# Optimization experiments

Hardware: AMD Instinct MI355X
Metric: run time of the kernel (lower is better)

The kernel has to match this reference:

```python
import jax, jax.numpy as jnp
import numpy as np

L, D, H, F_IN = 3, 256, 8, 5
HD = D // H
FF = 4 * D
EPS = 1e-5


def _layer_norm(x, g, b):
    mu = jnp.mean(x, axis=-1, keepdims=True)
    var = jnp.mean(jnp.square(x - mu), axis=-1, keepdims=True)
    return (x - mu) * jax.lax.rsqrt(var + EPS) * g + b


def setup_inputs() -> dict:
    key = jax.random.key(0)
    ks = jax.random.split(key, 20)
    s = 0.02
    inp = {
        'x': jax.random.normal(ks[0], (32, 512, F_IN), jnp.float32),
        'mask': jax.random.randint(ks[1], (32, 512), 0, 2) == 1,
        'Win': jax.random.normal(ks[2], (F_IN, D), jnp.float32) * s,
        'bin_': jnp.zeros((D,), jnp.float32),
        'Wq': jax.random.normal(ks[3], (L, D, D), jnp.float32) * s,
        'bq': jnp.zeros((L, D), jnp.float32),
        'Wk': jax.random.normal(ks[4], (L, D, D), jnp.float32) * s,
        'bk': jnp.zeros((L, D), jnp.float32),
        'Wv': jax.random.normal(ks[5], (L, D, D), jnp.float32) * s,
        'bv': jnp.zeros((L, D), jnp.float32),
        'Wo': jax.random.normal(ks[6], (L, D, D), jnp.float32) * s,
        'bo': jnp.zeros((L, D), jnp.float32),
        'g1': jnp.ones((L, D), jnp.float32),
        'b1': jnp.zeros((L, D), jnp.float32),
        'W1': jax.random.normal(ks[7], (L, D, FF), jnp.float32) * s,
        'c1': jnp.zeros((L, FF), jnp.float32),
        'W2': jax.random.normal(ks[8], (L, FF, D), jnp.float32) * s,
        'c2': jnp.zeros((L, D), jnp.float32),
        'g2': jnp.ones((L, D), jnp.float32),
        'b2': jnp.zeros((L, D), jnp.float32),
    }
    return inp


def reference(x, mask, Win, bin_, Wq, bq, Wk, bk, Wv, bv, Wo, bo, g1, b1, W1, c1, W2, c2, g2, b2):
    B, S, _ = x.shape
    scale = 1.0 / jnp.sqrt(jnp.float32(HD))
    h = x @ Win + bin_  # [B,S,D]
    kmask = mask[:, None, None, :]  # [B,1,1,S] key-padding mask
    for l in range(L):
        q = (h @ Wq[l] + bq[l]).reshape(B, S, H, HD).transpose(0, 2, 1, 3)
        k = (h @ Wk[l] + bk[l]).reshape(B, S, H, HD).transpose(0, 2, 1, 3)
        v = (h @ Wv[l] + bv[l]).reshape(B, S, H, HD).transpose(0, 2, 1, 3)
        scores = jnp.einsum('bhqd,bhkd->bhqk', q, k) * scale
        scores = jnp.where(kmask, -jnp.inf, scores)
        attn = jnp.nan_to_num(jax.nn.softmax(scores, axis=-1), nan=0.0)
        ao = jnp.einsum('bhqk,bhkd->bhqd', attn, v).transpose(0, 2, 1, 3).reshape(B, S, D)
        ao = ao @ Wo[l] + bo[l]
        h = _layer_norm(h + ao, g1[l], b1[l])
        ff = jax.nn.relu(h @ W1[l] + c1[l]) @ W2[l] + c2[l]
        h = _layer_norm(h + ff, g2[l], b2[l])
    return h
```

## Files before the change

### kernel.cpp

```cpp
#include <hip/hip_runtime.h>
#include <cstdint>

#define NLAYER 3
#define DMODEL 256
#define NHEAD 8
#define HEADD 32
#define FFDIM 1024
#define BATCH 32
#define SEQ 512
#define MTOK (BATCH*SEQ)

typedef __attribute__((ext_vector_type(8))) __bf16 bf16x8;
typedef __attribute__((ext_vector_type(4))) __bf16 bf16x4;
typedef __attribute__((ext_vector_type(4))) float f32x4;
typedef __attribute__((ext_vector_type(16))) float f32x16;

typedef __attribute__((address_space(1))) const uint8_t ga_t;
typedef __attribute__((address_space(3))) uint8_t la_t;
__device__ __forceinline__ void gll16(const void* g, void* l) {
    __builtin_amdgcn_global_load_lds((ga_t*)g, (la_t*)l, 16, 0, 0);
}

__global__ __launch_bounds__(256)
void prep_kernel(const float* __restrict__ Wq, const float* __restrict__ Wk,
                 const float* __restrict__ Wv, const float* __restrict__ Wo,
                 const float* __restrict__ W1, const float* __restrict__ W2,
                 const float* __restrict__ bq, const float* __restrict__ bk,
                 const float* __restrict__ bv,
                 __bf16* __restrict__ wqf, __bf16* __restrict__ wot,
                 __bf16* __restrict__ w1f, __bf16* __restrict__ w2f,
                 float* __restrict__ bqkv,
                 const float* __restrict__ x, const float* __restrict__ Win,
                 const float* __restrict__ bin, __bf16* __restrict__ h16)
{
    const int bid = blockIdx.x;
    const int tid = threadIdx.x;
    if (bid >= 2313) {
        const int m0 = (bid - 2313) * 8;
        const float bv_ = bin[tid];
#pragma unroll
        for (int p = 0; p < 8; ++p) {
            const int m = m0 + p;
            const float* xr = x + (size_t)m * 5;
            float acc = bv_;
#pragma unroll
            for (int k = 0; k < 5; ++k) acc += xr[k] * Win[k * DMODEL + tid];
            h16[(size_t)m * DMODEL + tid] = (__bf16)acc;
        }
        return;
    }
    if (bid >= 3 * 768) {
        int idx = (bid - 3 * 768) * 256 + tid;
        int l = idx / 768, j = idx % 768;
        float v = (j < 256) ? bq[l * 256 + j]
                : (j < 512) ? bk[l * 256 + j - 256]
                            : bv[l * 256 + j - 512];
        bqkv[idx] = v;
        return;
    }
    const int l = bid / 768;
    const int rr = bid % 768;
    __shared__ float tile[32][33];
    const int c = tid & 31, rbase = tid >> 5;

    if (rr < 192) {
        const int ty = rr >> 6;
        const int t = rr & 63;
        const float* src = (ty == 0 ? Wq : ty == 1 ? Wk : Wv) + (size_t)l * 65536;
        const int tk = t >> 3, tj = t & 7;
#pragma unroll
        for (int p = 0; p < 4; ++p) {
            int kr = rbase + p * 8;
            tile[kr][c] = src[(size_t)(tk * 32 + kr) * 256 + tj * 32 + c];
        }
        __syncthreads();
        if (tid < 128) {
            const int lane = tid & 63, ksl = tid >> 6;
            const int cl = lane & 31, kh = lane >> 5;
            bf16x8 v;
#pragma unroll
            for (int j = 0; j < 8; ++j) v[j] = (__bf16)tile[ksl * 16 + kh * 8 + j][cl];
            *(bf16x8*)(wqf + ((size_t)(((l * 8 + tj) * 3 + ty) * 16
                              + tk * 2 + ksl)) * 512 + lane * 8) = v;
        }
        return;
    }
    if (rr < 256) {
        const int t = rr - 192;
        const float* src = Wo + (size_t)l * 65536;
        __bf16* dst = wot + (size_t)l * 65536;
        const int tk = t >> 3, tj = t & 7;
#pragma unroll
        for (int p = 0; p < 4; ++p) {
            int kr = rbase + p * 8;
            tile[kr][c] = src[(size_t)(tk * 32 + kr) * 256 + tj * 32 + c];
        }
        __syncthreads();
#pragma unroll
        for (int p = 0; p < 4; ++p) {
            int nr = rbase + p * 8;
            dst[(size_t)(tj * 32 + nr) * 256 + tk * 32 + c] = (__bf16)tile[c][nr];
        }
        return;
    }
    const float* src; __bf16* dst; int N, KT, t;
    if (rr < 512) { t = rr - 256; src = W1 + (size_t)l * 262144;
                    dst = w1f + (size_t)l * 262144; N = 1024; KT = 8; }
    else          { t = rr - 512; src = W2 + (size_t)l * 262144;
                    dst = w2f + (size_t)l * 262144; N = 256;  KT = 32; }
    const int tn = N >> 5;
    const int tk = t / tn, tj = t % tn;
#pragma unroll
    for (int p = 0; p < 4; ++p) {
        int kr = rbase + p * 8;
        tile[kr][c] = src[(size_t)(tk * 32 + kr) * N + tj * 32 + c];
    }
    __syncthreads();
    if (tid < 128) {
        const int l_n = tid >> 2, k8 = tid & 3;
        const int n = tj * 32 + l_n;
        bf16x8 v;
#pragma unroll
        for (int j = 0; j < 8; ++j) v[j] = (__bf16)tile[k8 * 8 + j][l_n];
        *(bf16x8*)(dst + ((size_t)((n >> 4) * KT + tk) * 64 + k8 * 16 + (n & 15)) * 8) = v;
    }
}

__global__ __launch_bounds__(1024)
void attn_kernel(const __bf16* __restrict__ hA, const __bf16* __restrict__ wqf,
                 const float* __restrict__ bqkv, const int* __restrict__ mask,
                 __bf16* __restrict__ ao)
{
    __shared__ __bf16 Ks[512 * 40];
    __shared__ __bf16 Vt[32 * 520];
    __shared__ __attribute__((aligned(16))) __bf16 Un[3*16*512];
    __shared__ float maskadd[512];

    const int b = blockIdx.x >> 3;
    const int h = blockIdx.x & 7;
    const int t = threadIdx.x;
    const int lane = t & 63;
    const int wave = t >> 6;
    const int cl = lane & 31;
    const int kh = lane >> 5;
    const float scale = 0.17677669529663687f;

    {
        const __bf16* wsrc = wqf + (size_t)h * 24576;
#pragma unroll
        for (int p = 0; p < 3; ++p) {
            const int chunk = p * 1024 + t;
            gll16(wsrc + (size_t)chunk * 8, Un + (p * 1024 + wave * 64) * 8);
        }
    }
    if (t < 512) maskadd[t] = mask[b * SEQ + t] ? -1e30f : 0.f;
    __syncthreads();

    const int tok0 = wave * 32;
    const size_t arow = ((size_t)(b * SEQ + tok0 + cl)) * 256;
    f32x16 aQ, aK, aV;
#pragma unroll
    for (int i = 0; i < 16; ++i) { aQ[i] = 0.f; aK[i] = 0.f; aV[i] = 0.f; }
#pragma unroll
    for (int ks = 0; ks < 16; ++ks) {
        bf16x8 tf = *(const bf16x8*)(hA + arow + ks * 16 + kh * 8);
        bf16x8 wq = *(const bf16x8*)(Un + (0 * 16 + ks) * 512 + lane * 8);
        bf16x8 wk = *(const bf16x8*)(Un + (1 * 16 + ks) * 512 + lane * 8);
        bf16x8 wv = *(const bf16x8*)(Un + (2 * 16 + ks) * 512 + lane * 8);
        aQ = __builtin_amdgcn_mfma_f32_32x32x16_bf16(wq, tf, aQ, 0, 0, 0);
        aK = __builtin_amdgcn_mfma_f32_32x32x16_bf16(wk, tf, aK, 0, 0, 0);
        aV = __builtin_amdgcn_mfma_f32_32x32x16_bf16(wv, tf, aV, 0, 0, 0);
    }
#pragma unroll
    for (int r = 0; r < 16; ++r) {
        const int rdim = (r & 3) + 8 * (r >> 2) + 4 * kh;
        Ks[(tok0 + cl) * 40 + rdim] = (__bf16)(aK[r] + bqkv[256 + h * 32 + rdim]);
        Vt[rdim * 520 + tok0 + cl]  = (__bf16)(aV[r] + bqkv[512 + h * 32 + rdim]);
    }
    __syncthreads();

    __bf16* Pw = Un + wave * 1024;
#pragma unroll
    for (int r = 0; r < 16; ++r) {
        const int rdim = (r & 3) + 8 * (r >> 2) + 4 * kh;
        Pw[cl * 32 + rdim] = (__bf16)(aQ[r] + bqkv[h * 32 + rdim]);
    }
    bf16x8 qf0 = *(const bf16x8*)(Pw + cl * 32 + kh * 8);
    bf16x8 qf1 = *(const bf16x8*)(Pw + cl * 32 + 16 + kh * 8);
    __syncthreads();

    f32x16 oacc;
#pragma unroll
    for (int i = 0; i < 16; ++i) oacc[i] = 0.f;
    float lsum = 0.f;

    for (int kt = 0; kt < SEQ; kt += 32) {
        bf16x8 kf0 = *(const bf16x8*)(Ks + (kt + cl) * 40 + kh * 8);
        bf16x8 kf1 = *(const bf16x8*)(Ks + (kt + cl) * 40 + 16 + kh * 8);
        f32x16 s;
#pragma unroll
        for (int i = 0; i < 16; ++i) s[i] = 0.f;
        s = __builtin_amdgcn_mfma_f32_32x32x16_bf16(kf0, qf0, s, 0, 0, 0);
        s = __builtin_amdgcn_mfma_f32_32x32x16_bf16(kf1, qf1, s, 0, 0, 0);
        float pv[16];
#pragma unroll
        for (int g = 0; g < 4; ++g) {
            f32x4 mv = *(const f32x4*)(maskadd + kt + 8 * g + 4 * kh);
#pragma unroll
            for (int r = 0; r < 4; ++r) {
                float e = __expf(s[g * 4 + r] * scale + mv[r]);
                pv[g * 4 + r] = e;
                lsum += e;
            }
        }
#pragma unroll
        for (int g = 0; g < 4; ++g) {
            bf16x4 pb;
#pragma unroll
            for (int r = 0; r < 4; ++r) pb[r] = (__bf16)pv[g * 4 + r];
            *(bf16x4*)(Pw + cl * 32 + 8 * g + 4 * kh) = pb;
        }
        bf16x8 pf0 = *(const bf16x8*)(Pw + cl * 32 + kh * 8);
        bf16x8 pf1 = *(const bf16x8*)(Pw + cl * 32 + 16 + kh * 8);
        bf16x8 vf0 = *(const bf16x8*)(Vt + cl * 520 + kt + kh * 8);
        bf16x8 vf1 = *(const bf16x8*)(Vt + cl * 520 + kt + 16 + kh * 8);
        oacc = __builtin_amdgcn_mfma_f32_32x32x16_bf16(vf0, pf0, oacc, 0, 0, 0);
        oacc = __builtin_amdgcn_mfma_f32_32x32x16_bf16(vf1, pf1, oacc, 0, 0, 0);
    }

    lsum += __shfl_xor(lsum, 32);
    const float inv = (lsum > 0.f) ? 1.f / lsum : 0.f;
    __bf16* orow = ao + (size_t)(b * SEQ + tok0 + cl) * DMODEL + h * 32;
#pragma unroll
    for (int g = 0; g < 4; ++g) {
        bf16x4 w;
#pragma unroll
        for (int r = 0; r < 4; ++r) w[r] = (__bf16)(oacc[g * 4 + r] * inv);
        *(bf16x4*)(orow + 8 * g + 4 * kh) = w;
    }
}

template<int LAST>
__global__ __launch_bounds__(256, 4)
void gemm_ln_kernel(const __bf16* __restrict__ A, const __bf16* __restrict__ Bt,
                    const float* __restrict__ bias, const __bf16* __restrict__ res,
                    const float* __restrict__ g, const float* __restrict__ be,
                    __bf16* __restrict__ out16, float* __restrict__ out32, int K)
{
    __shared__ __bf16 As[32 * 64];
    __shared__ __bf16 Bs[256 * 64];
    __shared__ float red[32 * 8];
    const int tid = threadIdx.x;
    const int m0 = blockIdx.x * 32;
    const int lane = tid & 63;
    const int wave = tid >> 6;
    const int wn = wave * 64;
    const int fr = lane & 15;
    const int quad = lane >> 4;
    const int lr = lane >> 3;
    const int qg = (lane & 7) ^ lr;
    const int frs = fr & 7;

    const __bf16* Ab = A  + (size_t)(m0 + wave * 8 + lr) * K + qg * 8;
    const __bf16* Bb = Bt + (size_t)(wave * 64 + lr) * K + qg * 8;

    f32x4 acc[2][4];
#pragma unroll
    for (int i = 0; i < 2; ++i)
#pragma unroll
        for (int j = 0; j < 4; ++j)
#pragma unroll
            for (int r = 0; r < 4; ++r) acc[i][j][r] = 0.f;

    for (int k0 = 0; k0 < K; k0 += 64) {
        gll16(Ab + k0, As + wave * 512);
#pragma unroll
        for (int p = 0; p < 8; ++p)
            gll16(Bb + (size_t)p * 8 * K + k0, Bs + (wave * 8 + p) * 512);
        __syncthreads();
#pragma unroll
        for (int kk = 0; kk < 2; ++kk) {
            bf16x8 af[2], bfr[4];
#pragma unroll
            for (int i = 0; i < 2; ++i) {
                int row = i * 16 + fr;
                af[i] = *(const bf16x8*)(As + row * 64 + (((kk * 4 + quad) ^ frs) * 8));
            }
#pragma unroll
            for (int j = 0; j < 4; ++j) {
                int row = wn + j * 16 + fr;
                bfr[j] = *(const bf16x8*)(Bs + row * 64 + (((kk * 4 + quad) ^ frs) * 8));
            }
#pragma unroll
            for (int i = 0; i < 2; ++i)
#pragma unroll
                for (int j = 0; j < 4; ++j)
                    acc[i][j] = __builtin_amdgcn_mfma_f32_16x16x32_bf16(
                        af[i], bfr[j], acc[i][j], 0, 0, 0);
        }
        __syncthreads();
    }

    float bv[4];
#pragma unroll
    for (int j = 0; j < 4; ++j) bv[j] = bias[wn + j * 16 + fr];

#pragma unroll
    for (int i = 0; i < 2; ++i) {
#pragma unroll
        for (int r = 0; r < 4; ++r) {
            const int row = i * 16 + quad * 4 + r;
            float ps = 0.f, pq = 0.f;
#pragma unroll
            for (int j = 0; j < 4; ++j) {
                const int gc = wn + j * 16 + fr;
                float v = acc[i][j][r] + bv[j]
                        + (float)res[(size_t)(m0 + row) * DMODEL + gc];
                acc[i][j][r] = v;
                ps += v;
                pq += v * v;
            }
#pragma unroll
            for (int off = 1; off < 16; off <<= 1) {
                ps += __shfl_xor(ps, off, 64);
                pq += __shfl_xor(pq, off, 64);
            }
            if (fr == 0) {
                red[row * 8 + wave * 2]     = ps;
                red[row * 8 + wave * 2 + 1] = pq;
            }
        }
    }
    __syncthreads();

#pragma unroll
    for (int i = 0; i < 2; ++i) {
#pragma unroll
        for (int r = 0; r < 4; ++r) {
            const int row = i * 16 + quad * 4 + r;
            f32x4 a = *(const f32x4*)(red + row * 8);
            f32x4 b2 = *(const f32x4*)(red + row * 8 + 4);
            const float s  = a[0] + a[2] + b2[0] + b2[2];
            const float sq = a[1] + a[3] + b2[1] + b2[3];
            const float mu = s * (1.f / DMODEL);
            const float var = sq * (1.f / DMODEL) - mu * mu;
            const float rs = rsqrtf(var + 1e-5f);
#pragma unroll
            for (int j = 0; j < 4; ++j) {
                const int gc = wn + j * 16 + fr;
                float y = (acc[i][j][r] - mu) * rs * g[gc] + be[gc];
                if (LAST) out32[(size_t)(m0 + row) * DMODEL + gc] = y;
                else      out16[(size_t)(m0 + row) * DMODEL + gc] = (__bf16)y;
            }
        }
    }
}

template<int LAST>
__global__ __launch_bounds__(256, 3)
void ff_kernel(const __bf16* __restrict__ A, const __bf16* __restrict__ w1f,
               const float* __restrict__ c1, const __bf16* __restrict__ w2f,
               const float* __restrict__ c2, const __bf16* __restrict__ res,
               const float* __restrict__ g, const float* __restrict__ be,
               __bf16* __restrict__ out16, float* __restrict__ out32)
{
    __shared__ __attribute__((aligned(16))) __bf16 As[4][32 * 64];
    __shared__ __attribute__((aligned(16))) __bf16 P[32 * 136];
    __shared__ float c1s[1024];
    __shared__ float red[32 * 8];
    const int tid = threadIdx.x;
    const int lane = tid & 63;
    const int wave = tid >> 6;
    const int fr = lane & 15;
    const int quad = lane >> 4;
    const int m0 = blockIdx.x * 32;
    const int frs = fr & 7;

    {
        const int lr = lane >> 3, pos = lane & 7;
#pragma unroll
        for (int c4 = 0; c4 < 4; ++c4) {
            const int row = c4 * 8 + lr;
            const int gsw = pos ^ (row & 7);
            gll16(A + (size_t)(m0 + row) * 256 + wave * 64 + gsw * 8,
                  &As[wave][c4 * 8 * 64]);
        }
    }
    *(f32x4*)(c1s + tid * 4) = *(const f32x4*)(c1 + tid * 4);

    f32x4 acc2[2][4];
#pragma unroll
    for (int i = 0; i < 2; ++i)
#pragma unroll
        for (int j = 0; j < 4; ++j)
#pragma unroll
            for (int r = 0; r < 4; ++r) acc2[i][j][r] = 0.f;
    __syncthreads();

    for (int ch = 0; ch < 8; ++ch) {
        f32x4 acc1[2][2];
#pragma unroll
        for (int i = 0; i < 2; ++i)
#pragma unroll
            for (int j = 0; j < 2; ++j)
#pragma unroll
                for (int r = 0; r < 4; ++r) acc1[i][j][r] = 0.f;
#pragma unroll
        for (int ks = 0; ks < 8; ++ks) {
            bf16x8 af[2], bfr[2];
#pragma unroll
            for (int i = 0; i < 2; ++i)
                af[i] = *(const bf16x8*)(&As[ks >> 1][(i * 16 + fr) * 64
                         + ((((ks & 1) * 4 + quad) ^ frs) * 8)]);
#pragma unroll
            for (int j = 0; j < 2; ++j) {
                const int ntf = ch * 8 + wave * 2 + j;
                bfr[j] = *(const bf16x8*)(w1f + ((size_t)(ntf * 8 + ks) * 64 + lane) * 8);
            }
#pragma unroll
            for (int i = 0; i < 2; ++i)
#pragma unroll
                for (int j = 0; j < 2; ++j)
                    acc1[i][j] = __builtin_amdgcn_mfma_f32_16x16x32_bf16(
                        af[i], bfr[j], acc1[i][j], 0, 0, 0);
        }
#pragma unroll
        for (int j = 0; j < 2; ++j) {
            const float cb = c1s[ch * 128 + wave * 32 + j * 16 + fr];
#pragma unroll
            for (int i = 0; i < 2; ++i)
#pragma unroll
                for (int r = 0; r < 4; ++r) {
                    const int rowm = i * 16 + quad * 4 + r;
                    float v = fmaxf(acc1[i][j][r] + cb, 0.f);
                    P[rowm * 136 + wave * 32 + j * 16 + fr] = (__bf16)v;
                }
        }
        __syncthreads();
#pragma unroll
        for (int ks = 0; ks < 4; ++ks) {
            bf16x8 pf[2], wf[4];
#pragma unroll
            for (int i = 0; i < 2; ++i)
                pf[i] = *(const bf16x8*)(P + (i * 16 + fr) * 136 + ks * 32 + quad * 8);
#pragma unroll
            for (int j = 0; j < 4; ++j) {
                const int ntg = wave * 4 + j;
                const int kt = ch * 4 + ks;
                wf[j] = *(const bf16x8*)(w2f + ((size_t)(ntg * 32 + kt) * 64 + lane) * 8);
            }
#pragma unroll
            for (int i = 0; i < 2; ++i)
#pragma unroll
                for (int j = 0; j < 4; ++j)
                    acc2[i][j] = __builtin_amdgcn_mfma_f32_16x16x32_bf16(
                        pf[i], wf[j], acc2[i][j], 0, 0, 0);
        }
        __syncthreads();
    }

    const int wn = wave * 64;
    float bv[4];
#pragma unroll
    for (int j = 0; j < 4; ++j) bv[j] = c2[wn + j * 16 + fr];

#pragma unroll
    for (int i = 0; i < 2; ++i) {
#pragma unroll
        for (int r = 0; r < 4; ++r) {
            const int row = i * 16 + quad * 4 + r;
            float ps = 0.f, pq = 0.f;
#pragma unroll
            for (int j = 0; j < 4; ++j) {
                const int gc = wn + j * 16 + fr;
                float v = acc2[i][j][r] + bv[j]
                        + (float)res[(size_t)(m0 + row) * DMODEL + gc];
                acc2[i][j][r] = v;
                ps += v;
                pq += v * v;
            }
#pragma unroll
            for (int off = 1; off < 16; off <<= 1) {
                ps += __shfl_xor(ps, off, 64);
                pq += __shfl_xor(pq, off, 64);
            }
            if (fr == 0) {
                red[row * 8 + wave * 2]     = ps;
                red[row * 8 + wave * 2 + 1] = pq;
            }
        }
    }
    __syncthreads();

#pragma unroll
    for (int i = 0; i < 2; ++i) {
#pragma unroll
        for (int r = 0; r < 4; ++r) {
            const int row = i * 16 + quad * 4 + r;
            f32x4 a = *(const f32x4*)(red + row * 8);
            f32x4 b2 = *(const f32x4*)(red + row * 8 + 4);
            const float s  = a[0] + a[2] + b2[0] + b2[2];
            const float sq = a[1] + a[3] + b2[1] + b2[3];
            const float mu = s * (1.f / DMODEL);
            const float var = sq * (1.f / DMODEL) - mu * mu;
            const float rs = rsqrtf(var + 1e-5f);
#pragma unroll
            for (int j = 0; j < 4; ++j) {
                const int gc = wn + j * 16 + fr;
                float y = (acc2[i][j][r] - mu) * rs * g[gc] + be[gc];
                if (LAST) out32[(size_t)(m0 + row) * DMODEL + gc] = y;
                else      out16[(size_t)(m0 + row) * DMODEL + gc] = (__bf16)y;
            }
        }
    }
}

extern "C" void kernel_launch(void* const* d_in, const int* in_sizes, int n_in,
                              void* d_out, int out_size, void* d_ws, size_t ws_size,
                              hipStream_t stream)
{
    const float* x   = (const float*)d_in[0];
    const int*   mask= (const int*)d_in[1];
    const float* Win = (const float*)d_in[2];
    const float* bin = (const float*)d_in[3];
    const float* Wq  = (const float*)d_in[4];
    const float* bq  = (const float*)d_in[5];
    const float* Wk  = (const float*)d_in[6];
    const float* bk  = (const float*)d_in[7];
    const float* Wv  = (const float*)d_in[8];
    const float* bv  = (const float*)d_in[9];
    const float* Wo  = (const float*)d_in[10];
    const float* bo  = (const float*)d_in[11];
    const float* g1  = (const float*)d_in[12];
    const float* b1  = (const float*)d_in[13];
    const float* W1  = (const float*)d_in[14];
    const float* c1  = (const float*)d_in[15];
    const float* W2  = (const float*)d_in[16];
    const float* c2  = (const float*)d_in[17];
    const float* g2  = (const float*)d_in[18];
    const float* b2  = (const float*)d_in[19];

    char* ws = (char*)d_ws;
    size_t off = 0;
    auto alloc = [&](size_t bytes) -> void* {
        void* p = ws + off;
        off += (bytes + 255) & ~(size_t)255;
        return p;
    };
    __bf16* hA   = (__bf16*)alloc((size_t)MTOK * 256 * 2);
    __bf16* hB   = (__bf16*)alloc((size_t)MTOK * 256 * 2);
    __bf16* ao   = (__bf16*)alloc((size_t)MTOK * 256 * 2);
    __bf16* wqf  = (__bf16*)alloc((size_t)3 * 8 * 3 * 16 * 512 * 2);
    __bf16* wot  = (__bf16*)alloc((size_t)3 * 256 * 256 * 2);
    __bf16* w1f  = (__bf16*)alloc((size_t)3 * 1024 * 256 * 2);
    __bf16* w2f  = (__bf16*)alloc((size_t)3 * 256 * 1024 * 2);
    float*  bqkv = (float*)alloc((size_t)3 * 768 * 4);

    prep_kernel<<<dim3(2313 + MTOK / 8), dim3(256), 0, stream>>>(
        Wq, Wk, Wv, Wo, W1, W2, bq, bk, bv, wqf, wot, w1f, w2f, bqkv,
        x, Win, bin, hA);

    for (int l = 0; l < NLAYER; ++l) {
        attn_kernel<<<dim3(256), dim3(1024), 0, stream>>>(
            hA, wqf + (size_t)l * 8 * 3 * 16 * 512, bqkv + l * 768, mask, ao);
        gemm_ln_kernel<0><<<dim3(MTOK / 32), dim3(256), 0, stream>>>(
            ao, wot + (size_t)l * 65536, bo + l * 256, hA,
            g1 + l * 256, b1 + l * 256, hB, nullptr, 256);
        if (l == 2) {
            ff_kernel<1><<<dim3(MTOK / 32), dim3(256), 0, stream>>>(
                hB, w1f + (size_t)l * 262144, c1 + l * 1024,
                w2f + (size_t)l * 262144, c2 + l * 256, hB,
                g2 + l * 256, b2 + l * 256, nullptr, (float*)d_out);
        } else {
            ff_kernel<0><<<dim3(MTOK / 32), dim3(256), 0, stream>>>(
                hB, w1f + (size_t)l * 262144, c1 + l * 1024,
                w2f + (size_t)l * 262144, c2 + l * 256, hB,
                g2 + l * 256, b2 + l * 256, hA, nullptr);
        }
    }
}
```

Baseline: 364.9 us.

## Swap MFMA operand roles in FF kernel, double-buffer P, prefetch W2 fragments

The FF kernel now feeds the weights as the A operand and the activations as B, so each MFMA output lane holds four consecutive feature columns. This allows vectorized bf16x4/f32x4 stores for the hidden activations, bias, residual and LayerNorm output, and shortens the row reduction to two shuffles. P is double-buffered, which removes the trailing barrier in each chunk. W2 fragments for the whole chunk are loaded into registers up front. The added register pressure lowers the occupancy hint from 3 to 2 blocks, and the prep kernel's W1/W2 fragment layout is rewritten to match.

```diff
diff --git a/kernel.cpp b/kernel.cpp
--- a/kernel.cpp
+++ b/kernel.cpp
@@ -103,26 +103,27 @@
         }
         return;
     }
-    const float* src; __bf16* dst; int N, KT, t;
+    const float* src; int NN, tk, tj, t;
     if (rr < 512) { t = rr - 256; src = W1 + (size_t)l * 262144;
-                    dst = w1f + (size_t)l * 262144; N = 1024; KT = 8; }
+                    NN = 1024; tk = t >> 5; tj = t & 31; }
     else          { t = rr - 512; src = W2 + (size_t)l * 262144;
-                    dst = w2f + (size_t)l * 262144; N = 256;  KT = 32; }
-    const int tn = N >> 5;
-    const int tk = t / tn, tj = t % tn;
+                    NN = 256;  tk = t >> 3; tj = t & 7; }
 #pragma unroll
     for (int p = 0; p < 4; ++p) {
         int kr = rbase + p * 8;
-        tile[kr][c] = src[(size_t)(tk * 32 + kr) * N + tj * 32 + c];
+        tile[kr][c] = src[(size_t)(tk * 32 + kr) * NN + tj * 32 + c];
     }
     __syncthreads();
     if (tid < 128) {
-        const int l_n = tid >> 2, k8 = tid & 3;
-        const int n = tj * 32 + l_n;
+        const int sub = tid >> 6, lane = tid & 63;
+        const int fq = lane >> 4, ff = lane & 15;
         bf16x8 v;
 #pragma unroll
-        for (int j = 0; j < 8; ++j) v[j] = (__bf16)tile[k8 * 8 + j][l_n];
-        *(bf16x8*)(dst + ((size_t)((n >> 4) * KT + tk) * 64 + k8 * 16 + (n & 15)) * 8) = v;
+        for (int j = 0; j < 8; ++j) v[j] = (__bf16)tile[fq * 8 + j][sub * 16 + ff];
+        if (rr < 512)
+            *(bf16x8*)(w1f + ((size_t)(l * 64 + tj * 2 + sub) * 8 + tk) * 512 + lane * 8) = v;
+        else
+            *(bf16x8*)(w2f + ((size_t)(l * 16 + tj * 2 + sub) * 32 + tk) * 512 + lane * 8) = v;
     }
 }
 
@@ -357,15 +358,15 @@
 }
 
 template<int LAST>
-__global__ __launch_bounds__(256, 3)
-void ff_kernel(const __bf16* __restrict__ A, const __bf16* __restrict__ w1f,
-               const float* __restrict__ c1, const __bf16* __restrict__ w2f,
+__global__ __launch_bounds__(256, 2)
+void ff_kernel(const __bf16* __restrict__ A, const __bf16* __restrict__ w1A,
+               const float* __restrict__ c1, const __bf16* __restrict__ w2A,
                const float* __restrict__ c2, const __bf16* __restrict__ res,
                const float* __restrict__ g, const float* __restrict__ be,
                __bf16* __restrict__ out16, float* __restrict__ out32)
 {
     __shared__ __attribute__((aligned(16))) __bf16 As[4][32 * 64];
-    __shared__ __attribute__((aligned(16))) __bf16 P[32 * 136];
+    __shared__ __attribute__((aligned(16))) __bf16 P[2][32 * 136];
     __shared__ float c1s[1024];
     __shared__ float red[32 * 8];
     const int tid = threadIdx.x;
@@ -374,7 +375,6 @@
     const int fr = lane & 15;
     const int quad = lane >> 4;
     const int m0 = blockIdx.x * 32;
-    const int frs = fr & 7;
 
     {
         const int lr = lane >> 3, pos = lane & 7;
@@ -388,16 +388,25 @@
     }
     *(f32x4*)(c1s + tid * 4) = *(const f32x4*)(c1 + tid * 4);
 
-    f32x4 acc2[2][4];
-#pragma unroll
-    for (int i = 0; i < 2; ++i)
-#pragma unroll
-        for (int j = 0; j < 4; ++j)
-#pragma unroll
-            for (int r = 0; r < 4; ++r) acc2[i][j][r] = 0.f;
-    __syncthreads();
-
+    f32x4 acc2[4][2];
+#pragma unroll
+    for (int jj = 0; jj < 4; ++jj)
+#pragma unroll
+        for (int tt = 0; tt < 2; ++tt)
+#pragma unroll
+            for (int r = 0; r < 4; ++r) acc2[jj][tt][r] = 0.f;
+    __syncthreads();
+
+#pragma unroll 2
     for (int ch = 0; ch < 8; ++ch) {
+        bf16x8 w2r[4][4];
+#pragma unroll
+        for (int jj = 0; jj < 4; ++jj)
+#pragma unroll
+            for (int ks = 0; ks < 4; ++ks) {
+                const int dt = wave * 4 + jj, kt = ch * 4 + ks;
+                w2r[jj][ks] = *(const bf16x8*)(w2A + ((size_t)(dt * 32 + kt) * 64 + lane) * 8);
+            }
         f32x4 acc1[2][2];
 #pragma unroll
         for (int i = 0; i < 2; ++i)
@@ -407,109 +416,111 @@
                 for (int r = 0; r < 4; ++r) acc1[i][j][r] = 0.f;
 #pragma unroll
         for (int ks = 0; ks < 8; ++ks) {
-            bf16x8 af[2], bfr[2];
-#pragma unroll
-            for (int i = 0; i < 2; ++i)
-                af[i] = *(const bf16x8*)(&As[ks >> 1][(i * 16 + fr) * 64
-                         + ((((ks & 1) * 4 + quad) ^ frs) * 8)]);
-#pragma unroll
-            for (int j = 0; j < 2; ++j) {
-                const int ntf = ch * 8 + wave * 2 + j;
-                bfr[j] = *(const bf16x8*)(w1f + ((size_t)(ntf * 8 + ks) * 64 + lane) * 8);
-            }
+            bf16x8 w1r[2], tf[2];
+#pragma unroll
+            for (int i = 0; i < 2; ++i) {
+                const int ft = ch * 8 + wave * 2 + i;
+                w1r[i] = *(const bf16x8*)(w1A + ((size_t)(ft * 8 + ks) * 64 + lane) * 8);
+            }
+#pragma unroll
+            for (int j = 0; j < 2; ++j)
+                tf[j] = *(const bf16x8*)(&As[ks >> 1][(j * 16 + fr) * 64
+                          + ((((ks & 1) * 4 + quad) ^ (fr & 7)) * 8)]);
 #pragma unroll
             for (int i = 0; i < 2; ++i)
 #pragma unroll
                 for (int j = 0; j < 2; ++j)
                     acc1[i][j] = __builtin_amdgcn_mfma_f32_16x16x32_bf16(
-                        af[i], bfr[j], acc1[i][j], 0, 0, 0);
-        }
-#pragma unroll
-        for (int j = 0; j < 2; ++j) {
-            const float cb = c1s[ch * 128 + wave * 32 + j * 16 + fr];
-#pragma unroll
-            for (int i = 0; i < 2; ++i)
-#pragma unroll
-                for (int r = 0; r < 4; ++r) {
-                    const int rowm = i * 16 + quad * 4 + r;
-                    float v = fmaxf(acc1[i][j][r] + cb, 0.f);
-                    P[rowm * 136 + wave * 32 + j * 16 + fr] = (__bf16)v;
-                }
+                        w1r[i], tf[j], acc1[i][j], 0, 0, 0);
+        }
+#pragma unroll
+        for (int i = 0; i < 2; ++i) {
+            f32x4 cb = *(const f32x4*)(c1s + ch * 128 + wave * 32 + i * 16 + quad * 4);
+#pragma unroll
+            for (int j = 0; j < 2; ++j) {
+                bf16x4 pb;
+#pragma unroll
+                for (int r = 0; r < 4; ++r)
+                    pb[r] = (__bf16)fmaxf(acc1[i][j][r] + cb[r], 0.f);
+                *(bf16x4*)(&P[ch & 1][(j * 16 + fr) * 136 + wave * 32 + i * 16 + quad * 4]) = pb;
+            }
         }
         __syncthreads();
 #pragma unroll
         for (int ks = 0; ks < 4; ++ks) {
-            bf16x8 pf[2], wf[4];
-#pragma unroll
-            for (int i = 0; i < 2; ++i)
-                pf[i] = *(const bf16x8*)(P + (i * 16 + fr) * 136 + ks * 32 + quad * 8);
-#pragma unroll
-            for (int j = 0; j < 4; ++j) {
-                const int ntg = wave * 4 + j;
-                const int kt = ch * 4 + ks;
-                wf[j] = *(const bf16x8*)(w2f + ((size_t)(ntg * 32 + kt) * 64 + lane) * 8);
-            }
-#pragma unroll
-            for (int i = 0; i < 2; ++i)
-#pragma unroll
-                for (int j = 0; j < 4; ++j)
-                    acc2[i][j] = __builtin_amdgcn_mfma_f32_16x16x32_bf16(
-                        pf[i], wf[j], acc2[i][j], 0, 0, 0);
-        }
-        __syncthreads();
-    }
-
-    const int wn = wave * 64;
-    float bv[4];
-#pragma unroll
-    for (int j = 0; j < 4; ++j) bv[j] = c2[wn + j * 16 + fr];
-
-#pragma unroll
-    for (int i = 0; i < 2; ++i) {
-#pragma unroll
-        for (int r = 0; r < 4; ++r) {
-            const int row = i * 16 + quad * 4 + r;
-            float ps = 0.f, pq = 0.f;
-#pragma unroll
-            for (int j = 0; j < 4; ++j) {
-                const int gc = wn + j * 16 + fr;
-                float v = acc2[i][j][r] + bv[j]
-                        + (float)res[(size_t)(m0 + row) * DMODEL + gc];
-                acc2[i][j][r] = v;
-                ps += v;
-                pq += v * v;
-            }
-#pragma unroll
-            for (int off = 1; off < 16; off <<= 1) {
-                ps += __shfl_xor(ps, off, 64);
-                pq += __shfl_xor(pq, off, 64);
-            }
-            if (fr == 0) {
-                red[row * 8 + wave * 2]     = ps;
-                red[row * 8 + wave * 2 + 1] = pq;
-            }
-        }
-    }
-    __syncthreads();
-
-#pragma unroll
-    for (int i = 0; i < 2; ++i) {
-#pragma unroll
-        for (int r = 0; r < 4; ++r) {
-            const int row = i * 16 + quad * 4 + r;
-            f32x4 a = *(const f32x4*)(red + row * 8);
-            f32x4 b2 = *(const f32x4*)(red + row * 8 + 4);
-            const float s  = a[0] + a[2] + b2[0] + b2[2];
-            const float sq = a[1] + a[3] + b2[1] + b2[3];
-            const float mu = s * (1.f / DMODEL);
-            const float var = sq * (1.f / DMODEL) - mu * mu;
-            const float rs = rsqrtf(var + 1e-5f);
-#pragma unroll
-            for (int j = 0; j < 4; ++j) {
-                const int gc = wn + j * 16 + fr;
-                float y = (acc2[i][j][r] - mu) * rs * g[gc] + be[gc];
-                if (LAST) out32[(size_t)(m0 + row) * DMODEL + gc] = y;
-                else      out16[(size_t)(m0 + row) * DMODEL + gc] = (__bf16)y;
+            bf16x8 pf[2];
+#pragma unroll
+            for (int tt = 0; tt < 2; ++tt)
+                pf[tt] = *(const bf16x8*)(&P[ch & 1][(tt * 16 + fr) * 136 + ks * 32 + quad * 8]);
+#pragma unroll
+            for (int jj = 0; jj < 4; ++jj)
+#pragma unroll
+                for (int tt = 0; tt < 2; ++tt)
+                    acc2[jj][tt] = __builtin_amdgcn_mfma_f32_16x16x32_bf16(
+                        w2r[jj][ks], pf[tt], acc2[jj][tt], 0, 0, 0);
+        }
+    }
+
+    float ps0 = 0.f, pq0 = 0.f, ps1 = 0.f, pq1 = 0.f;
+#pragma unroll
+    for (int jj = 0; jj < 4; ++jj) {
+        f32x4 cb = *(const f32x4*)(c2 + wave * 64 + jj * 16 + quad * 4);
+#pragma unroll
+        for (int tt = 0; tt < 2; ++tt) {
+            bf16x4 rv = *(const bf16x4*)(res + (size_t)(m0 + tt * 16 + fr) * DMODEL
+                                         + wave * 64 + jj * 16 + quad * 4);
+#pragma unroll
+            for (int r = 0; r < 4; ++r) {
+                float v = acc2[jj][tt][r] + cb[r] + (float)rv[r];
+                acc2[jj][tt][r] = v;
+                if (tt == 0) { ps0 += v; pq0 += v * v; }
+                else         { ps1 += v; pq1 += v * v; }
+            }
+        }
+    }
+    ps0 += __shfl_xor(ps0, 16); ps0 += __shfl_xor(ps0, 32);
+    pq0 += __shfl_xor(pq0, 16); pq0 += __shfl_xor(pq0, 32);
+    ps1 += __shfl_xor(ps1, 16); ps1 += __shfl_xor(ps1, 32);
+    pq1 += __shfl_xor(pq1, 16); pq1 += __shfl_xor(pq1, 32);
+    if (quad == 0) {
+        red[fr * 8 + wave * 2]            = ps0;
+        red[fr * 8 + wave * 2 + 1]        = pq0;
+        red[(16 + fr) * 8 + wave * 2]     = ps1;
+        red[(16 + fr) * 8 + wave * 2 + 1] = pq1;
+    }
+    __syncthreads();
+    float mu[2], rs_[2];
+#pragma unroll
+    for (int tt = 0; tt < 2; ++tt) {
+        const int tok = tt * 16 + fr;
+        f32x4 a = *(const f32x4*)(red + tok * 8);
+        f32x4 b2 = *(const f32x4*)(red + tok * 8 + 4);
+        const float s  = a[0] + a[2] + b2[0] + b2[2];
+        const float sq = a[1] + a[3] + b2[1] + b2[3];
+        mu[tt] = s * (1.f / DMODEL);
+        const float var = sq * (1.f / DMODEL) - mu[tt] * mu[tt];
+        rs_[tt] = rsqrtf(var + 1e-5f);
+    }
+#pragma unroll
+    for (int jj = 0; jj < 4; ++jj) {
+        f32x4 gv = *(const f32x4*)(g  + wave * 64 + jj * 16 + quad * 4);
+        f32x4 bv = *(const f32x4*)(be + wave * 64 + jj * 16 + quad * 4);
+#pragma unroll
+        for (int tt = 0; tt < 2; ++tt) {
+            const size_t base = (size_t)(m0 + tt * 16 + fr) * DMODEL
+                              + wave * 64 + jj * 16 + quad * 4;
+            if (LAST) {
+                f32x4 y;
+#pragma unroll
+                for (int r = 0; r < 4; ++r)
+                    y[r] = (acc2[jj][tt][r] - mu[tt]) * rs_[tt] * gv[r] + bv[r];
+                *(f32x4*)(out32 + base) = y;
+            } else {
+                bf16x4 y;
+#pragma unroll
+                for (int r = 0; r < 4; ++r)
+                    y[r] = (__bf16)((acc2[jj][tt][r] - mu[tt]) * rs_[tt] * gv[r] + bv[r]);
+                *(bf16x4*)(out16 + base) = y;
             }
         }
     }
```

After: 345.1 us. 5.4% less time.
